# Kernel optimization log

Hardware: AMD Instinct MI355X
Metric: run time of the kernel (lower is better)

## Reference

```python
import jax, jax.numpy as jnp
import numpy as np

TOPK = 2  # matches init_kwargs topk


def setup_inputs() -> dict:
    key = jax.random.key(0)
    k1, k2 = jax.random.split(key)
    T, D, E = 32768, 4096, 16
    hidden_states = jax.random.normal(k1, (T, D), dtype=jnp.float32)
    wg_weight = jax.random.normal(k2, (E, D), dtype=jnp.float32) * 0.02  # [num_experts, hidden]
    return {"hidden_states": hidden_states, "wg_weight": wg_weight}


def reference(hidden_states, wg_weight):
    # logits = hidden_states @ wg.T  -> [T, E], computed in fp32 as in the torch module
    logits = jnp.einsum("td,ed->te", hidden_states.astype(jnp.float32), wg_weight.astype(jnp.float32))
    gates = jax.nn.softmax(logits, axis=-1)  # [T, E]
    topk_weights, topk_indices = jax.lax.top_k(gates, TOPK)  # [T, K] each
    topk_weights = topk_weights / jnp.sum(topk_weights, axis=-1, keepdims=True)
    return topk_indices, topk_weights.astype(hidden_states.dtype)
```

## Files before the change

kernel.cpp:

```cpp
#include <hip/hip_runtime.h>
#include <math.h>

#define T_TOKENS 32768
#define HID      4096
#define NEXP     16
#define MT       4
#define WAVES    4
#define D4       (HID / 4)
#define KI       (D4 / 64)

typedef float f32x4 __attribute__((ext_vector_type(4)));

__global__ __launch_bounds__(256) void moe_gate_kernel(
    const float* __restrict__ h,
    const float* __restrict__ w,
    float* __restrict__ out)
{
    __shared__ f32x4 sw[3][NEXP][64];

    const int lane = threadIdx.x & 63;
    const int wv   = threadIdx.x >> 6;
    const int t0   = (blockIdx.x * WAVES + wv) * MT;

    const f32x4* __restrict__ w4 = reinterpret_cast<const f32x4*>(w);
    const f32x4* hrow[MT];
    #pragma unroll
    for (int t = 0; t < MT; ++t)
        hrow[t] = reinterpret_cast<const f32x4*>(h + (size_t)(t0 + t) * HID);

    float acc[MT * NEXP];
    #pragma unroll
    for (int i = 0; i < MT * NEXP; ++i) acc[i] = 0.0f;

#define STAGE(b, ki_) do {                                                    \
        _Pragma("unroll")                                                     \
        for (int j = 0; j < 4; ++j) {                                         \
            const int e_ = wv * 4 + j;                                        \
            const f32x4* gsrc = w4 + (size_t)e_ * D4 + (ki_) * 64 + lane;     \
            __builtin_amdgcn_global_load_lds(                                 \
                (const __attribute__((address_space(1))) void*)gsrc,          \
                (__attribute__((address_space(3))) void*)&sw[b][e_][0],       \
                16, 0, 0);                                                    \
        }                                                                     \
    } while (0)

#define LOADH(dst, ki_) do {                                                  \
        const int d4_ = (ki_) * 64 + lane;                                    \
        _Pragma("unroll")                                                     \
        for (int t = 0; t < MT; ++t)                                          \
            dst[t] = __builtin_nontemporal_load(&hrow[t][d4_]);               \
    } while (0)

#define COMPUTE(b, hreg) do {                                                 \
        _Pragma("unroll")                                                     \
        for (int e_ = 0; e_ < NEXP; ++e_) {                                   \
            f32x4 wvv = sw[b][e_][lane];                                      \
            _Pragma("unroll")                                                 \
            for (int t = 0; t < MT; ++t) {                                    \
                float a = acc[t * NEXP + e_];                                 \
                a = fmaf(hreg[t][0], wvv[0], a);                              \
                a = fmaf(hreg[t][1], wvv[1], a);                              \
                a = fmaf(hreg[t][2], wvv[2], a);                              \
                a = fmaf(hreg[t][3], wvv[3], a);                              \
                acc[t * NEXP + e_] = a;                                       \
            }                                                                 \
        }                                                                     \
    } while (0)

    f32x4 hv[MT], hn[MT];
    STAGE(0, 0);
    LOADH(hv, 0);
    STAGE(1, 1);
    LOADH(hn, 1);
    asm volatile("s_waitcnt vmcnt(4)" ::: "memory");
    __builtin_amdgcn_s_barrier();
    asm volatile("" ::: "memory");
    __builtin_amdgcn_sched_barrier(0);

    int cur = 0;
    for (int ki = 0; ki < KI - 2; ++ki) {
        const int stg = (cur >= 1) ? cur - 1 : cur + 2;
        STAGE(stg, ki + 2);
        f32x4 h2[MT];
        LOADH(h2, ki + 2);
        COMPUTE(cur, hv);
        #pragma unroll
        for (int t = 0; t < MT; ++t) { hv[t] = hn[t]; hn[t] = h2[t]; }
        asm volatile("s_waitcnt vmcnt(8)" ::: "memory");
        __builtin_amdgcn_s_barrier();
        asm volatile("" ::: "memory");
        __builtin_amdgcn_sched_barrier(0);
        cur = (cur >= 2) ? 0 : cur + 1;
    }

    COMPUTE(cur, hv);
    asm volatile("s_waitcnt vmcnt(0)" ::: "memory");
    __builtin_amdgcn_s_barrier();
    asm volatile("" ::: "memory");
    __builtin_amdgcn_sched_barrier(0);
    cur = (cur >= 2) ? 0 : cur + 1;
    COMPUTE(cur, hn);

    #pragma unroll
    for (int b = 32; b >= 1; b >>= 1) {
        const bool hi = (lane & b) != 0;
        #pragma unroll
        for (int j = 0; j < b; ++j) {
            float lo_v = acc[j];
            float hi_v = acc[j + b];
            float keepv = hi ? hi_v : lo_v;
            float sendv = hi ? lo_v : hi_v;
            acc[j] = keepv + __shfl_xor(sendv, b, 64);
        }
    }
    const float logit = acc[0];

    const int eidx = lane & 15;
    float m1 = logit; int i1 = eidx;
    #pragma unroll
    for (int s = 1; s < 16; s <<= 1) {
        float ov = __shfl_xor(m1, s, 64);
        int   oi = __shfl_xor(i1, s, 64);
        if (ov > m1 || (ov == m1 && oi < i1)) { m1 = ov; i1 = oi; }
    }
    float masked = (eidx == i1) ? -INFINITY : logit;
    float m2 = masked; int i2 = eidx;
    #pragma unroll
    for (int s = 1; s < 16; s <<= 1) {
        float ov = __shfl_xor(m2, s, 64);
        int   oi = __shfl_xor(i2, s, 64);
        if (ov > m2 || (ov == m2 && oi < i2)) { m2 = ov; i2 = oi; }
    }

    if (eidx == 0) {
        const int t = t0 + (lane >> 4);
        const float r  = expf(m2 - m1);
        const float s  = 1.0f / (1.0f + r);
        float2* oidx = reinterpret_cast<float2*>(out);
        float2* owt  = reinterpret_cast<float2*>(out + 2 * T_TOKENS);
        oidx[t] = make_float2((float)i1, (float)i2);
        owt[t]  = make_float2(s, r * s);
    }
#undef STAGE
#undef LOADH
#undef COMPUTE
}

extern "C" void kernel_launch(void* const* d_in, const int* in_sizes, int n_in,
                              void* d_out, int out_size, void* d_ws, size_t ws_size,
                              hipStream_t stream) {
    const float* h = (const float*)d_in[0];
    const float* w = (const float*)d_in[1];
    float* out = (float*)d_out;

    const int blocks = T_TOKENS / (MT * WAVES);
    moe_gate_kernel<<<blocks, 256, 0, stream>>>(h, w, out);
}
```

Before: 118.0 us.

## Process eight tokens per wave with a double-buffered weight pipeline

Each wave now handles eight tokens instead of four. Every gate-weight vector read from LDS is reused across twice as many tokens, and the grid has half as many blocks. The triple-buffered, two-ahead prefetch is reduced to a double-buffered, one-ahead prefetch. The launch bound requests two blocks per CU. The accumulator array grows to 128 floats per lane, raising register pressure, and the shallower prefetch may expose more latency on a kernel that is limited by memory bandwidth.

```diff
diff --git a/kernel.cpp b/kernel.cpp
--- a/kernel.cpp
+++ b/kernel.cpp
@@ -4,19 +4,19 @@
 #define T_TOKENS 32768
 #define HID      4096
 #define NEXP     16
-#define MT       4
+#define MT       8
 #define WAVES    4
 #define D4       (HID / 4)
 #define KI       (D4 / 64)
 
 typedef float f32x4 __attribute__((ext_vector_type(4)));
 
-__global__ __launch_bounds__(256) void moe_gate_kernel(
+__global__ __launch_bounds__(256, 2) void moe_gate_kernel(
     const float* __restrict__ h,
     const float* __restrict__ w,
     float* __restrict__ out)
 {
-    __shared__ f32x4 sw[3][NEXP][64];
+    __shared__ f32x4 sw[2][NEXP][64];
 
     const int lane = threadIdx.x & 63;
     const int wv   = threadIdx.x >> 6;
@@ -67,83 +67,85 @@
         }                                                                     \
     } while (0)
 
-    f32x4 hv[MT], hn[MT];
+    f32x4 hv[MT];
     STAGE(0, 0);
     LOADH(hv, 0);
-    STAGE(1, 1);
-    LOADH(hn, 1);
-    asm volatile("s_waitcnt vmcnt(4)" ::: "memory");
+    asm volatile("s_waitcnt vmcnt(8)" ::: "memory");
     __builtin_amdgcn_s_barrier();
     asm volatile("" ::: "memory");
     __builtin_amdgcn_sched_barrier(0);
 
     int cur = 0;
-    for (int ki = 0; ki < KI - 2; ++ki) {
-        const int stg = (cur >= 1) ? cur - 1 : cur + 2;
-        STAGE(stg, ki + 2);
-        f32x4 h2[MT];
-        LOADH(h2, ki + 2);
+    for (int ki = 0; ki < KI - 1; ++ki) {
+        STAGE(cur ^ 1, ki + 1);
+        f32x4 hn[MT];
+        LOADH(hn, ki + 1);
         COMPUTE(cur, hv);
         #pragma unroll
-        for (int t = 0; t < MT; ++t) { hv[t] = hn[t]; hn[t] = h2[t]; }
+        for (int t = 0; t < MT; ++t) hv[t] = hn[t];
         asm volatile("s_waitcnt vmcnt(8)" ::: "memory");
         __builtin_amdgcn_s_barrier();
         asm volatile("" ::: "memory");
         __builtin_amdgcn_sched_barrier(0);
-        cur = (cur >= 2) ? 0 : cur + 1;
+        cur ^= 1;
     }
+    COMPUTE(cur, hv);
 
-    COMPUTE(cur, hv);
-    asm volatile("s_waitcnt vmcnt(0)" ::: "memory");
-    __builtin_amdgcn_s_barrier();
-    asm volatile("" ::: "memory");
-    __builtin_amdgcn_sched_barrier(0);
-    cur = (cur >= 2) ? 0 : cur + 1;
-    COMPUTE(cur, hn);
+#define BUTTERFLY(base) do {                                                  \
+        _Pragma("unroll")                                                     \
+        for (int b = 32; b >= 1; b >>= 1) {                                   \
+            const bool hi_ = (lane & b) != 0;                                 \
+            _Pragma("unroll")                                                 \
+            for (int j = 0; j < b; ++j) {                                     \
+                float lo_v = acc[(base) + j];                                 \
+                float hi_v = acc[(base) + j + b];                             \
+                float keepv = hi_ ? hi_v : lo_v;                              \
+                float sendv = hi_ ? lo_v : hi_v;                              \
+                acc[(base) + j] = keepv + __shfl_xor(sendv, b, 64);           \
+            }                                                                 \
+        }                                                                     \
+    } while (0)
 
-    #pragma unroll
-    for (int b = 32; b >= 1; b >>= 1) {
-        const bool hi = (lane & b) != 0;
-        #pragma unroll
-        for (int j = 0; j < b; ++j) {
-            float lo_v = acc[j];
-            float hi_v = acc[j + b];
-            float keepv = hi ? hi_v : lo_v;
-            float sendv = hi ? lo_v : hi_v;
-            acc[j] = keepv + __shfl_xor(sendv, b, 64);
-        }
-    }
-    const float logit = acc[0];
+    BUTTERFLY(0);
+    BUTTERFLY(64);
+    const float logit0 = acc[0];
+    const float logit1 = acc[64];
 
     const int eidx = lane & 15;
-    float m1 = logit; int i1 = eidx;
-    #pragma unroll
-    for (int s = 1; s < 16; s <<= 1) {
-        float ov = __shfl_xor(m1, s, 64);
-        int   oi = __shfl_xor(i1, s, 64);
-        if (ov > m1 || (ov == m1 && oi < i1)) { m1 = ov; i1 = oi; }
-    }
-    float masked = (eidx == i1) ? -INFINITY : logit;
-    float m2 = masked; int i2 = eidx;
-    #pragma unroll
-    for (int s = 1; s < 16; s <<= 1) {
-        float ov = __shfl_xor(m2, s, 64);
-        int   oi = __shfl_xor(i2, s, 64);
-        if (ov > m2 || (ov == m2 && oi < i2)) { m2 = ov; i2 = oi; }
-    }
+#define TOP2_WRITE(logit_, tok_) do {                                         \
+        float m1 = (logit_); int i1 = eidx;                                   \
+        _Pragma("unroll")                                                     \
+        for (int s = 1; s < 16; s <<= 1) {                                    \
+            float ov = __shfl_xor(m1, s, 64);                                 \
+            int   oi = __shfl_xor(i1, s, 64);                                 \
+            if (ov > m1 || (ov == m1 && oi < i1)) { m1 = ov; i1 = oi; }       \
+        }                                                                     \
+        float masked = (eidx == i1) ? -INFINITY : (logit_);                   \
+        float m2 = masked; int i2 = eidx;                                     \
+        _Pragma("unroll")                                                     \
+        for (int s = 1; s < 16; s <<= 1) {                                    \
+            float ov = __shfl_xor(m2, s, 64);                                 \
+            int   oi = __shfl_xor(i2, s, 64);                                 \
+            if (ov > m2 || (ov == m2 && oi < i2)) { m2 = ov; i2 = oi; }       \
+        }                                                                     \
+        if (eidx == 0) {                                                      \
+            const float r_ = expf(m2 - m1);                                   \
+            const float s_ = 1.0f / (1.0f + r_);                              \
+            float2* oidx = reinterpret_cast<float2*>(out);                    \
+            float2* owt  = reinterpret_cast<float2*>(out + 2 * T_TOKENS);     \
+            oidx[tok_] = make_float2((float)i1, (float)i2);                   \
+            owt[tok_]  = make_float2(s_, r_ * s_);                            \
+        }                                                                     \
+    } while (0)
 
-    if (eidx == 0) {
-        const int t = t0 + (lane >> 4);
-        const float r  = expf(m2 - m1);
-        const float s  = 1.0f / (1.0f + r);
-        float2* oidx = reinterpret_cast<float2*>(out);
-        float2* owt  = reinterpret_cast<float2*>(out + 2 * T_TOKENS);
-        oidx[t] = make_float2((float)i1, (float)i2);
-        owt[t]  = make_float2(s, r * s);
-    }
+    TOP2_WRITE(logit0, t0 + (lane >> 4));
+    TOP2_WRITE(logit1, t0 + 4 + (lane >> 4));
+
 #undef STAGE
 #undef LOADH
 #undef COMPUTE
+#undef BUTTERFLY
+#undef TOP2_WRITE
 }
 
 extern "C" void kernel_launch(void* const* d_in, const int* in_sizes, int n_in,
```

Result: no change. 117.9 us (-0.1%).

## Stage half of gate weights in LDS per block with deeper register prefetch

Applied to the files above, without the earlier changes.

Replaces the triple-buffered per-chunk weight staging with two large LDS stages, each holding half the hidden dimension for all experts, so only two block barriers are needed instead of one per chunk. Doubles the block to 8 waves, which amortizes weight staging over more tokens. Hidden-state loads are prefetched three chunks ahead in a four-register rotation. The costs are 128KB of LDS per block, which limits occupancy, higher register pressure, and a stall at the midpoint restage.

```diff
diff --git a/kernel.cpp b/kernel.cpp
--- a/kernel.cpp
+++ b/kernel.cpp
@@ -2,59 +2,60 @@
 #include <math.h>
 
 #define T_TOKENS 32768
+#define NEXP     16
 #define HID      4096
-#define NEXP     16
 #define MT       4
-#define WAVES    4
+#define WAVES    8
 #define D4       (HID / 4)
-#define KI       (D4 / 64)
+#define HALF     (D4 / 2)
+#define NC       (HALF / 64)
 
 typedef float f32x4 __attribute__((ext_vector_type(4)));
 
-__global__ __launch_bounds__(256) void moe_gate_kernel(
+__global__ __launch_bounds__(512, 2) void moe_gate_kernel(
     const float* __restrict__ h,
     const float* __restrict__ w,
     float* __restrict__ out)
 {
-    __shared__ f32x4 sw[3][NEXP][64];
+    __shared__ f32x4 sw[NEXP][HALF];
 
     const int lane = threadIdx.x & 63;
     const int wv   = threadIdx.x >> 6;
-    const int t0   = (blockIdx.x * WAVES + wv) * MT;
-
+    const int t0   = blockIdx.x * (MT * WAVES) + wv * MT;
+    const int t0u  = __builtin_amdgcn_readfirstlane(t0);
+    const f32x4* __restrict__ hb =
+        reinterpret_cast<const f32x4*>(h + (size_t)t0u * HID);
     const f32x4* __restrict__ w4 = reinterpret_cast<const f32x4*>(w);
-    const f32x4* hrow[MT];
-    #pragma unroll
-    for (int t = 0; t < MT; ++t)
-        hrow[t] = reinterpret_cast<const f32x4*>(h + (size_t)(t0 + t) * HID);
 
     float acc[MT * NEXP];
     #pragma unroll
     for (int i = 0; i < MT * NEXP; ++i) acc[i] = 0.0f;
 
-#define STAGE(b, ki_) do {                                                    \
+#define STAGE(kh_) do {                                                       \
         _Pragma("unroll")                                                     \
-        for (int j = 0; j < 4; ++j) {                                         \
-            const int e_ = wv * 4 + j;                                        \
-            const f32x4* gsrc = w4 + (size_t)e_ * D4 + (ki_) * 64 + lane;     \
+        for (int j = 0; j < 16; ++j) {                                        \
+            const int e_ = 2 * wv + (j >> 3);                                 \
+            const int c_ = j & 7;                                             \
+            const f32x4* gsrc =                                               \
+                w4 + (size_t)e_ * D4 + (kh_) * HALF + c_ * 64 + lane;         \
             __builtin_amdgcn_global_load_lds(                                 \
                 (const __attribute__((address_space(1))) void*)gsrc,          \
-                (__attribute__((address_space(3))) void*)&sw[b][e_][0],       \
+                (__attribute__((address_space(3))) void*)&sw[e_][c_ * 64],    \
                 16, 0, 0);                                                    \
         }                                                                     \
     } while (0)
 
-#define LOADH(dst, ki_) do {                                                  \
-        const int d4_ = (ki_) * 64 + lane;                                    \
+#define LOADH(dst, g_) do {                                                   \
+        const int d4_ = (g_) * 64 + lane;                                     \
         _Pragma("unroll")                                                     \
         for (int t = 0; t < MT; ++t)                                          \
-            dst[t] = __builtin_nontemporal_load(&hrow[t][d4_]);               \
+            dst[t] = __builtin_nontemporal_load(hb + (size_t)t * D4 + d4_);   \
     } while (0)
 
-#define COMPUTE(b, hreg) do {                                                 \
+#define COMPUTE(l_, hreg) do {                                                \
         _Pragma("unroll")                                                     \
         for (int e_ = 0; e_ < NEXP; ++e_) {                                   \
-            f32x4 wvv = sw[b][e_][lane];                                      \
+            f32x4 wvv = sw[e_][(l_) * 64 + lane];                             \
             _Pragma("unroll")                                                 \
             for (int t = 0; t < MT; ++t) {                                    \
                 float a = acc[t * NEXP + e_];                                 \
@@ -67,49 +68,56 @@
         }                                                                     \
     } while (0)
 
-    f32x4 hv[MT], hn[MT];
-    STAGE(0, 0);
-    LOADH(hv, 0);
-    STAGE(1, 1);
-    LOADH(hn, 1);
-    asm volatile("s_waitcnt vmcnt(4)" ::: "memory");
+#define GROUP(A, B, C, D, g_, l_) do {                                        \
+        LOADH(D, (g_) + 3); COMPUTE((l_) + 0, A);                             \
+        LOADH(A, (g_) + 4); COMPUTE((l_) + 1, B);                             \
+        LOADH(B, (g_) + 5); COMPUTE((l_) + 2, C);                             \
+        LOADH(C, (g_) + 6); COMPUTE((l_) + 3, D);                             \
+    } while (0)
+
+    f32x4 bA[MT], bB[MT], bC[MT], bD[MT];
+
+    STAGE(0);
+    __builtin_amdgcn_sched_barrier(0);
+    LOADH(bA, 0);
+    LOADH(bB, 1);
+    LOADH(bC, 2);
+    __builtin_amdgcn_sched_barrier(0);
+    asm volatile("s_waitcnt vmcnt(12)" ::: "memory");
     __builtin_amdgcn_s_barrier();
     asm volatile("" ::: "memory");
     __builtin_amdgcn_sched_barrier(0);
 
-    int cur = 0;
-    for (int ki = 0; ki < KI - 2; ++ki) {
-        const int stg = (cur >= 1) ? cur - 1 : cur + 2;
-        STAGE(stg, ki + 2);
-        f32x4 h2[MT];
-        LOADH(h2, ki + 2);
-        COMPUTE(cur, hv);
-        #pragma unroll
-        for (int t = 0; t < MT; ++t) { hv[t] = hn[t]; hn[t] = h2[t]; }
-        asm volatile("s_waitcnt vmcnt(8)" ::: "memory");
-        __builtin_amdgcn_s_barrier();
-        asm volatile("" ::: "memory");
-        __builtin_amdgcn_sched_barrier(0);
-        cur = (cur >= 2) ? 0 : cur + 1;
-    }
+    #pragma unroll 1
+    for (int c = 0; c < NC; c += 4)
+        GROUP(bA, bB, bC, bD, c, c);
 
-    COMPUTE(cur, hv);
+    asm volatile("s_waitcnt lgkmcnt(0)" ::: "memory");
+    __builtin_amdgcn_s_barrier();
+    asm volatile("" ::: "memory");
+    STAGE(1);
+    __builtin_amdgcn_sched_barrier(0);
     asm volatile("s_waitcnt vmcnt(0)" ::: "memory");
     __builtin_amdgcn_s_barrier();
     asm volatile("" ::: "memory");
     __builtin_amdgcn_sched_barrier(0);
-    cur = (cur >= 2) ? 0 : cur + 1;
-    COMPUTE(cur, hn);
+
+    GROUP(bA, bB, bC, bD, 8, 0);
+    LOADH(bD, 15);
+    COMPUTE(4, bA);
+    COMPUTE(5, bB);
+    COMPUTE(6, bC);
+    COMPUTE(7, bD);
 
     #pragma unroll
     for (int b = 32; b >= 1; b >>= 1) {
-        const bool hi = (lane & b) != 0;
+        const bool hi_ = (lane & b) != 0;
         #pragma unroll
         for (int j = 0; j < b; ++j) {
             float lo_v = acc[j];
             float hi_v = acc[j + b];
-            float keepv = hi ? hi_v : lo_v;
-            float sendv = hi ? lo_v : hi_v;
+            float keepv = hi_ ? hi_v : lo_v;
+            float sendv = hi_ ? lo_v : hi_v;
             acc[j] = keepv + __shfl_xor(sendv, b, 64);
         }
     }
@@ -144,6 +152,7 @@
 #undef STAGE
 #undef LOADH
 #undef COMPUTE
+#undef GROUP
 }
 
 extern "C" void kernel_launch(void* const* d_in, const int* in_sizes, int n_in,
@@ -154,5 +163,5 @@
     float* out = (float*)d_out;
 
     const int blocks = T_TOKENS / (MT * WAVES);
-    moe_gate_kernel<<<blocks, 256, 0, stream>>>(h, w, out);
+    moe_gate_kernel<<<blocks, 512, 0, stream>>>(h, w, out);
 }
```

Result: slower. 198.7 us (+68.3%).
